# Optimization experiments

Hardware: AMD Instinct MI355X
Metric: run time of the kernel (lower is better)

## Reference

```python
import jax, jax.numpy as jnp
import numpy as np

EMBED_DIM = 1024
NUM_HEADS = 16
D_K = EMBED_DIM // NUM_HEADS


def setup_inputs() -> dict:
    key = jax.random.key(0)
    ks = jax.random.split(key, 5)
    s = 1.0 / np.sqrt(EMBED_DIM)  # roughly match nn.Linear init scale
    return {
        "x": jax.random.normal(ks[0], (2, 2048, EMBED_DIM), dtype=jnp.float32),
        "wq": jax.random.normal(ks[1], (EMBED_DIM, EMBED_DIM), dtype=jnp.float32) * s,
        "wk": jax.random.normal(ks[2], (EMBED_DIM, EMBED_DIM), dtype=jnp.float32) * s,
        "wv": jax.random.normal(ks[3], (EMBED_DIM, EMBED_DIM), dtype=jnp.float32) * s,
        "wo": jax.random.normal(ks[4], (EMBED_DIM, EMBED_DIM), dtype=jnp.float32) * s,
    }


def reference(x, wq, wk, wv, wo):
    b, s, e = x.shape
    # nn.Linear(bias=False): y = x @ W.T
    def split_heads(t):
        return t.reshape(b, s, NUM_HEADS, D_K).transpose(0, 2, 1, 3)  # [b,h,s,d]
    q = split_heads(x @ wq.T)
    k = split_heads(x @ wk.T)
    v = split_heads(x @ wv.T)
    scores = jnp.einsum("bhqd,bhkd->bhqk", q, k) / jnp.sqrt(jnp.float32(D_K))
    attn = jax.nn.softmax(scores, axis=-1)
    out = jnp.einsum("bhqk,bhkd->bhqd", attn, v)  # [b,h,s,d]
    out = out.transpose(0, 2, 1, 3).reshape(b, s, e)
    return out @ wo.T
```

## Files before the change

kernel.cpp:

```cpp
#include <hip/hip_runtime.h>
#include <stdint.h>

typedef unsigned short u16;
typedef float f32x4 __attribute__((ext_vector_type(4)));
typedef __bf16 bf16x8 __attribute__((ext_vector_type(8)));
typedef short s16x4 __attribute__((ext_vector_type(4)));

__device__ __forceinline__ u16 f2bf(float f) {
  union { float f; uint32_t u; } c; c.f = f;
  uint32_t u = c.u;
  u += 0x7fffu + ((u >> 16) & 1u);
  return (u16)(u >> 16);
}

__device__ __forceinline__ uint32_t pkbf(float a, float b) {
  union { float f; uint32_t u; } ua, ub; ua.f = a; ub.f = b;
  return __builtin_amdgcn_perm(ub.u, ua.u, 0x07060302u);
}

#define GLOAD_LDS16(g, l)                                                              \
  __builtin_amdgcn_global_load_lds((__attribute__((address_space(1))) void*)(g),       \
                                   (__attribute__((address_space(3))) void*)(l), 16, 0, 0)

__global__ __launch_bounds__(256) void cvt_all(const float* __restrict__ x,
                                               const float* __restrict__ wq,
                                               const float* __restrict__ wk,
                                               const float* __restrict__ wv,
                                               const float* __restrict__ wo,
                                               u16* __restrict__ xb,
                                               u16* __restrict__ wqkvb,
                                               u16* __restrict__ wob) {
  int bx = blockIdx.x;
  const float* src;
  u16* dst;
  int i;
  if (bx < 4096) {
    src = x; dst = xb; i = bx * 256 + threadIdx.x;
  } else {
    int r = bx - 4096;
    int w = r >> 10;
    i = (r & 1023) * 256 + threadIdx.x;
    if (w == 0)      { src = wq; dst = wqkvb; }
    else if (w == 1) { src = wk; dst = wqkvb + 1048576; }
    else if (w == 2) { src = wv; dst = wqkvb + 2097152; }
    else             { src = wo; dst = wob; }
  }
  const float4 v = ((const float4*)src)[i];
  ushort4 o;
  o.x = f2bf(v.x); o.y = f2bf(v.y); o.z = f2bf(v.z); o.w = f2bf(v.w);
  ((ushort4*)dst)[i] = o;
}

__global__ __launch_bounds__(256) void gemm_qkv(const u16* __restrict__ A,
                                                const u16* __restrict__ B,
                                                u16* __restrict__ QKb,
                                                u16* __restrict__ Vt) {
  const int K = 1024;
  __shared__ __align__(16) u16 sA[128 * 64];
  __shared__ __align__(16) u16 sB[128 * 64];
  const int tid = threadIdx.x;
  const int lane = tid & 63;
  const int wave = tid >> 6;
  const int quad = lane >> 4, l16 = lane & 15;
  const int wm = (wave >> 1) * 64, wn = (wave & 1) * 64;
  const int bm = blockIdx.y * 128, bn = blockIdx.x * 128;

  f32x4 acc[4][4];
#pragma unroll
  for (int i = 0; i < 4; i++)
#pragma unroll
    for (int j = 0; j < 4; j++) acc[i][j] = (f32x4){0.f, 0.f, 0.f, 0.f};

  for (int k0 = 0; k0 < K; k0 += 64) {
#pragma unroll
    for (int k2 = 0; k2 < 4; k2++) {
      int c = k2 * 256 + tid;
      int row = c >> 3, c8 = (c & 7) ^ (row & 7);
      GLOAD_LDS16(A + (size_t)(bm + row) * K + k0 + c8 * 8, (char*)sA + c * 16);
      GLOAD_LDS16(B + (size_t)(bn + row) * K + k0 + c8 * 8, (char*)sB + c * 16);
    }
    __syncthreads();
    bf16x8 af[4][2], bfr[4][2];
#pragma unroll
    for (int mt = 0; mt < 4; mt++)
#pragma unroll
      for (int kh = 0; kh < 2; kh++) {
        int ra = wm + mt * 16 + l16;
        af[mt][kh] = *(const bf16x8*)&sA[ra * 64 + (((kh * 4 + quad) ^ (ra & 7)) * 8)];
        int rb = wn + mt * 16 + l16;
        bfr[mt][kh] = *(const bf16x8*)&sB[rb * 64 + (((kh * 4 + quad) ^ (rb & 7)) * 8)];
      }
#pragma unroll
    for (int mt = 0; mt < 4; mt++)
#pragma unroll
      for (int nt = 0; nt < 4; nt++) {
        acc[mt][nt] = __builtin_amdgcn_mfma_f32_16x16x32_bf16(af[mt][0], bfr[nt][0], acc[mt][nt], 0, 0, 0);
        acc[mt][nt] = __builtin_amdgcn_mfma_f32_16x16x32_bf16(af[mt][1], bfr[nt][1], acc[mt][nt], 0, 0, 0);
      }
    __syncthreads();
  }

  if (blockIdx.x < 16) {
    const float qs = (blockIdx.x < 8) ? 0.18033688011f : 1.0f;
#pragma unroll
    for (int mt = 0; mt < 4; mt++)
#pragma unroll
      for (int nt = 0; nt < 4; nt++)
#pragma unroll
        for (int r = 0; r < 4; r++) {
          int row = bm + wm + mt * 16 + quad * 4 + r;
          int col = bn + wn + nt * 16 + l16;
          QKb[(size_t)row * 2048 + col] = f2bf(acc[mt][nt][r] * qs);
        }
  } else {
#pragma unroll
    for (int mt = 0; mt < 4; mt++)
#pragma unroll
      for (int nt = 0; nt < 4; nt++) {
        int hd = (bn - 2048) + wn + nt * 16 + l16;
        int tok = bm + wm + mt * 16 + quad * 4;
        ushort4 o;
        o.x = f2bf(acc[mt][nt][0]);
        o.y = f2bf(acc[mt][nt][1]);
        o.z = f2bf(acc[mt][nt][2]);
        o.w = f2bf(acc[mt][nt][3]);
        *(ushort4*)&Vt[(size_t)hd * 4096 + tok] = o;
      }
  }
}

__global__ __launch_bounds__(256, 2) void attn_fwd(const u16* __restrict__ QKb,
                                                   const u16* __restrict__ Vt,
                                                   u16* __restrict__ O) {
  const int bx = blockIdx.x;
  const int qt = bx >> 5;
  const int h  = (bx >> 1) & 15;
  const int b  = bx & 1;
  const int tid = threadIdx.x;
  const int lane = tid & 63;
  const int wave = tid >> 6;
  const int quad = lane >> 4, l16 = lane & 15;

  __shared__ __align__(16) u16 smem[16384];
  u16* sK0 = smem;
  u16* sK1 = smem + 4096;
  u16* sV0 = smem + 8192;
  u16* sV1 = smem + 12288;

  const int tok0 = b * 2048;
  const int q0 = qt * 128;
  const int colh = h * 64;

#pragma unroll
  for (int k2 = 0; k2 < 2; k2++) {
    int c = k2 * 256 + tid;
    int row = c >> 3, c8 = (c & 7) ^ (row & 7);
    GLOAD_LDS16(QKb + (size_t)(tok0 + q0 + row) * 2048 + colh + c8 * 8,
                (char*)sK1 + c * 16);
    GLOAD_LDS16(QKb + (size_t)(tok0 + q0 + 64 + row) * 2048 + colh + c8 * 8,
                (char*)sV1 + c * 16);
    GLOAD_LDS16(QKb + (size_t)(tok0 + row) * 2048 + 1024 + colh + c8 * 8,
                (char*)sK0 + c * 16);
    GLOAD_LDS16(Vt + (size_t)(colh + row) * 4096 + tok0 + c8 * 8,
                (char*)sV0 + c * 16);
  }
  __syncthreads();

  const u16* qreg = (wave < 2) ? sK1 : sV1;
  bf16x8 aq[2][2];
#pragma unroll
  for (int sub = 0; sub < 2; sub++)
#pragma unroll
    for (int kh = 0; kh < 2; kh++) {
      int r64 = (wave & 1) * 32 + sub * 16 + l16;
      aq[sub][kh] = *(const bf16x8*)&qreg[r64 * 64 + (((kh * 4 + quad) ^ (r64 & 7)) * 8)];
    }
  __syncthreads();

  f32x4 oacc[2][4];
  float lsum[2] = {0.f, 0.f};
#pragma unroll
  for (int sub = 0; sub < 2; sub++)
#pragma unroll
    for (int db = 0; db < 4; db++) oacc[sub][db] = (f32x4){0.f, 0.f, 0.f, 0.f};

  int p = 0;
  for (int it = 0; it < 32; ++it) {
    u16* sKc = p ? sK1 : sK0;
    u16* sVc = p ? sV1 : sV0;
    if (it < 31) {
      u16* sKn = p ? sK0 : sK1;
      u16* sVn = p ? sV0 : sV1;
      const int nkv = (it + 1) * 64;
#pragma unroll
      for (int k2 = 0; k2 < 2; k2++) {
        int c = k2 * 256 + tid;
        int row = c >> 3, c8 = (c & 7) ^ (row & 7);
        GLOAD_LDS16(QKb + (size_t)(tok0 + nkv + row) * 2048 + 1024 + colh + c8 * 8,
                    (char*)sKn + c * 16);
        GLOAD_LDS16(Vt + (size_t)(colh + row) * 4096 + tok0 + nkv + c8 * 8,
                    (char*)sVn + c * 16);
      }
    }

    bf16x8 kf[4][2];
#pragma unroll
    for (int nt = 0; nt < 4; nt++)
#pragma unroll
      for (int kh = 0; kh < 2; kh++) {
        int rr = nt * 16 + l16;
        kf[nt][kh] = *(const bf16x8*)&sKc[rr * 64 + (((kh * 4 + quad) ^ (rr & 7)) * 8)];
      }
    s16x4 vf[4][4];
#pragma unroll
    for (int db = 0; db < 4; db++)
#pragma unroll
      for (int nt = 0; nt < 4; nt++) {
        int row = db * 16 + l16;
        int c16 = (nt * 2 + (quad >> 1)) ^ (row & 7);
        vf[db][nt] = *(const s16x4*)&sVc[row * 64 + c16 * 8 + (quad & 1) * 4];
      }

#pragma unroll
    for (int sub = 0; sub < 2; sub++) {
      float e[4][4];
#pragma unroll
      for (int nt = 0; nt < 4; nt++) {
        f32x4 c = (f32x4){0.f, 0.f, 0.f, 0.f};
        c = __builtin_amdgcn_mfma_f32_16x16x32_bf16(kf[nt][0], aq[sub][0], c, 0, 0, 0);
        c = __builtin_amdgcn_mfma_f32_16x16x32_bf16(kf[nt][1], aq[sub][1], c, 0, 0, 0);
#pragma unroll
        for (int r = 0; r < 4; r++) e[nt][r] = __builtin_amdgcn_exp2f(c[r]);
        lsum[sub] += (e[nt][0] + e[nt][1]) + (e[nt][2] + e[nt][3]);
      }
#pragma unroll
      for (int nt = 0; nt < 4; nt++) {
        union { uint32_t u[2]; s16x4 v; } bb;
        bb.u[0] = pkbf(e[nt][0], e[nt][1]);
        bb.u[1] = pkbf(e[nt][2], e[nt][3]);
#pragma unroll
        for (int db = 0; db < 4; db++)
          oacc[sub][db] = __builtin_amdgcn_mfma_f32_16x16x16bf16_1k(vf[db][nt], bb.v, oacc[sub][db], 0, 0, 0);
      }
    }
    __syncthreads();
    p ^= 1;
  }

#pragma unroll
  for (int sub = 0; sub < 2; sub++) {
    float v = lsum[sub];
    v += __shfl_xor(v, 16, 64);
    v += __shfl_xor(v, 32, 64);
    lsum[sub] = 1.0f / v;
  }

  u16* sT = smem + wave * 2176;
#pragma unroll
  for (int sub = 0; sub < 2; sub++)
#pragma unroll
    for (int db = 0; db < 4; db++)
#pragma unroll
      for (int r = 0; r < 4; r++)
        sT[(sub * 16 + l16) * 68 + db * 16 + quad * 4 + r] = f2bf(oacc[sub][db][r] * lsum[sub]);
#pragma unroll
  for (int k = 0; k < 4; k++) {
    int qrow = k * 8 + (lane >> 3);
    int cch = lane & 7;
    uint4 vrow = *(const uint4*)&sT[qrow * 68 + cch * 8];
    int tokr = tok0 + q0 + wave * 32 + qrow;
    *(uint4*)&O[(size_t)tokr * 1024 + colh + cch * 8] = vrow;
  }
}

__global__ __launch_bounds__(256) void gemm_out(const u16* __restrict__ A,
                                                const u16* __restrict__ B,
                                                float* __restrict__ C) {
  const int N = 1024, K = 1024;
  __shared__ __align__(16) u16 sA[128 * 64];
  __shared__ __align__(16) u16 sB[64 * 64];
  const int tid = threadIdx.x;
  const int lane = tid & 63;
  const int wave = tid >> 6;
  const int quad = lane >> 4, l16 = lane & 15;
  const int wm = (wave >> 1) * 64, wn = (wave & 1) * 32;
  const int bm = blockIdx.y * 128, bn = blockIdx.x * 64;

  f32x4 acc[4][2];
#pragma unroll
  for (int i = 0; i < 4; i++)
#pragma unroll
    for (int j = 0; j < 2; j++) acc[i][j] = (f32x4){0.f, 0.f, 0.f, 0.f};

  for (int k0 = 0; k0 < K; k0 += 64) {
#pragma unroll
    for (int k2 = 0; k2 < 4; k2++) {
      int c = k2 * 256 + tid;
      int row = c >> 3, c8 = (c & 7) ^ (row & 7);
      GLOAD_LDS16(A + (size_t)(bm + row) * K + k0 + c8 * 8, (char*)sA + c * 16);
    }
#pragma unroll
    for (int k2 = 0; k2 < 2; k2++) {
      int c = k2 * 256 + tid;
      int row = c >> 3, c8 = (c & 7) ^ (row & 7);
      GLOAD_LDS16(B + (size_t)(bn + row) * K + k0 + c8 * 8, (char*)sB + c * 16);
    }
    __syncthreads();
    bf16x8 af[4][2], bfr[2][2];
#pragma unroll
    for (int mt = 0; mt < 4; mt++)
#pragma unroll
      for (int kh = 0; kh < 2; kh++) {
        int ra = wm + mt * 16 + l16;
        af[mt][kh] = *(const bf16x8*)&sA[ra * 64 + (((kh * 4 + quad) ^ (ra & 7)) * 8)];
      }
#pragma unroll
    for (int nt = 0; nt < 2; nt++)
#pragma unroll
      for (int kh = 0; kh < 2; kh++) {
        int rb = wn + nt * 16 + l16;
        bfr[nt][kh] = *(const bf16x8*)&sB[rb * 64 + (((kh * 4 + quad) ^ (rb & 7)) * 8)];
      }
#pragma unroll
    for (int mt = 0; mt < 4; mt++)
#pragma unroll
      for (int nt = 0; nt < 2; nt++) {
        acc[mt][nt] = __builtin_amdgcn_mfma_f32_16x16x32_bf16(af[mt][0], bfr[nt][0], acc[mt][nt], 0, 0, 0);
        acc[mt][nt] = __builtin_amdgcn_mfma_f32_16x16x32_bf16(af[mt][1], bfr[nt][1], acc[mt][nt], 0, 0, 0);
      }
    __syncthreads();
  }

#pragma unroll
  for (int mt = 0; mt < 4; mt++)
#pragma unroll
    for (int nt = 0; nt < 2; nt++)
#pragma unroll
      for (int r = 0; r < 4; r++) {
        int row = bm + wm + mt * 16 + quad * 4 + r;
        int col = bn + wn + nt * 16 + l16;
        C[(size_t)row * N + col] = acc[mt][nt][r];
      }
}

extern "C" void kernel_launch(void* const* d_in, const int* in_sizes, int n_in,
                              void* d_out, int out_size, void* d_ws, size_t ws_size,
                              hipStream_t stream) {
  const float* x  = (const float*)d_in[0];
  const float* wq = (const float*)d_in[1];
  const float* wk = (const float*)d_in[2];
  const float* wv = (const float*)d_in[3];
  const float* wo = (const float*)d_in[4];
  float* out = (float*)d_out;
  char* ws = (char*)d_ws;
  const size_t MB = 1u << 20;

  u16* xb    = (u16*)(ws);
  u16* wqkvb = (u16*)(ws + 8 * MB);
  u16* wob   = (u16*)(ws + 14 * MB);
  u16* QKb   = (u16*)(ws + 16 * MB);
  u16* Vtb   = (u16*)(ws + 32 * MB);
  u16* Ob    = xb;

  cvt_all<<<8192, 256, 0, stream>>>(x, wq, wk, wv, wo, xb, wqkvb, wob);

  gemm_qkv<<<dim3(24, 32), 256, 0, stream>>>(xb, wqkvb, QKb, Vtb);

  attn_fwd<<<512, 256, 0, stream>>>(QKb, Vtb, Ob);

  gemm_out<<<dim3(16, 32), 256, 0, stream>>>(Ob, wob, out);
}
```

Baseline: 186.5 us.

## Triple-buffer LDS pipelines in GEMMs and attention with async load waits

Both GEMMs now use a 3-stage LDS ring with 32-wide K slices, prefetching two stages ahead. Each stage waits on a partial vmcnt and issues a single barrier, replacing the load-then-syncthreads double sync per iteration. The attention kernel gets the same treatment: a 3-deep K/V ring, a dedicated Q buffer, and s_setprio raised around MFMA groups. The goal is to hide global-to-LDS latency behind compute. The cost is more LDS per block, which may reduce occupancy, and correctness now depends on the hand-counted vmcnt values and on the ordering implied by the single barrier.

```diff
diff --git a/kernel.cpp b/kernel.cpp
--- a/kernel.cpp
+++ b/kernel.cpp
@@ -51,13 +51,13 @@
   ((ushort4*)dst)[i] = o;
 }
 
-__global__ __launch_bounds__(256) void gemm_qkv(const u16* __restrict__ A,
-                                                const u16* __restrict__ B,
-                                                u16* __restrict__ QKb,
-                                                u16* __restrict__ Vt) {
+__global__ __launch_bounds__(256, 3) void gemm_qkv(const u16* __restrict__ A,
+                                                   const u16* __restrict__ B,
+                                                   u16* __restrict__ QKb,
+                                                   u16* __restrict__ Vt) {
   const int K = 1024;
-  __shared__ __align__(16) u16 sA[128 * 64];
-  __shared__ __align__(16) u16 sB[128 * 64];
+  __shared__ __align__(16) u16 sA[3 * 4096];
+  __shared__ __align__(16) u16 sB[3 * 4096];
   const int tid = threadIdx.x;
   const int lane = tid & 63;
   const int wave = tid >> 6;
@@ -71,34 +71,54 @@
 #pragma unroll
     for (int j = 0; j < 4; j++) acc[i][j] = (f32x4){0.f, 0.f, 0.f, 0.f};
 
-  for (int k0 = 0; k0 < K; k0 += 64) {
-#pragma unroll
-    for (int k2 = 0; k2 < 4; k2++) {
-      int c = k2 * 256 + tid;
-      int row = c >> 3, c8 = (c & 7) ^ (row & 7);
-      GLOAD_LDS16(A + (size_t)(bm + row) * K + k0 + c8 * 8, (char*)sA + c * 16);
-      GLOAD_LDS16(B + (size_t)(bn + row) * K + k0 + c8 * 8, (char*)sB + c * 16);
-    }
-    __syncthreads();
-    bf16x8 af[4][2], bfr[4][2];
+#define QKV_STAGE(t, bi)                                                           \
+  {                                                                                \
+    const int k0s = (t) * 32;                                                      \
+    char* dA = (char*)(sA + (bi) * 4096);                                          \
+    char* dB = (char*)(sB + (bi) * 4096);                                          \
+    _Pragma("unroll")                                                              \
+    for (int k2 = 0; k2 < 2; k2++) {                                               \
+      int u = k2 * 256 + tid;                                                      \
+      int row = u >> 2, c4 = (u & 3) ^ (row & 3);                                  \
+      GLOAD_LDS16(A + (size_t)(bm + row) * K + k0s + c4 * 8, dA + u * 16);         \
+      GLOAD_LDS16(B + (size_t)(bn + row) * K + k0s + c4 * 8, dB + u * 16);         \
+    }                                                                              \
+  }
+
+  QKV_STAGE(0, 0);
+  QKV_STAGE(1, 1);
+
+  int cur = 0, stg = 2;
+  for (int T = 0; T < 32; ++T) {
+    if (T < 31) asm volatile("s_waitcnt vmcnt(4)" ::: "memory");
+    else        asm volatile("s_waitcnt vmcnt(0)" ::: "memory");
+    __builtin_amdgcn_s_barrier();
+    asm volatile("" ::: "memory");
+    if (T < 30) QKV_STAGE(T + 2, stg);
+
+    const u16* cA = sA + cur * 4096;
+    const u16* cB = sB + cur * 4096;
+    bf16x8 af[4], bfr[4];
+#pragma unroll
+    for (int mt = 0; mt < 4; mt++) {
+      int ra = wm + mt * 16 + l16;
+      af[mt] = *(const bf16x8*)&cA[ra * 32 + ((quad ^ (ra & 3)) * 8)];
+    }
+#pragma unroll
+    for (int nt = 0; nt < 4; nt++) {
+      int rb = wn + nt * 16 + l16;
+      bfr[nt] = *(const bf16x8*)&cB[rb * 32 + ((quad ^ (rb & 3)) * 8)];
+    }
 #pragma unroll
     for (int mt = 0; mt < 4; mt++)
 #pragma unroll
-      for (int kh = 0; kh < 2; kh++) {
-        int ra = wm + mt * 16 + l16;
-        af[mt][kh] = *(const bf16x8*)&sA[ra * 64 + (((kh * 4 + quad) ^ (ra & 7)) * 8)];
-        int rb = wn + mt * 16 + l16;
-        bfr[mt][kh] = *(const bf16x8*)&sB[rb * 64 + (((kh * 4 + quad) ^ (rb & 7)) * 8)];
-      }
-#pragma unroll
-    for (int mt = 0; mt < 4; mt++)
-#pragma unroll
-      for (int nt = 0; nt < 4; nt++) {
-        acc[mt][nt] = __builtin_amdgcn_mfma_f32_16x16x32_bf16(af[mt][0], bfr[nt][0], acc[mt][nt], 0, 0, 0);
-        acc[mt][nt] = __builtin_amdgcn_mfma_f32_16x16x32_bf16(af[mt][1], bfr[nt][1], acc[mt][nt], 0, 0, 0);
-      }
-    __syncthreads();
-  }
+      for (int nt = 0; nt < 4; nt++)
+        acc[mt][nt] = __builtin_amdgcn_mfma_f32_16x16x32_bf16(af[mt], bfr[nt], acc[mt][nt], 0, 0, 0);
+
+    cur = (cur == 2) ? 0 : cur + 1;
+    stg = (stg == 2) ? 0 : stg + 1;
+  }
+#undef QKV_STAGE
 
   if (blockIdx.x < 16) {
     const float qs = (blockIdx.x < 8) ? 0.18033688011f : 1.0f;
@@ -141,41 +161,46 @@
   const int wave = tid >> 6;
   const int quad = lane >> 4, l16 = lane & 15;
 
-  __shared__ __align__(16) u16 smem[16384];
-  u16* sK0 = smem;
-  u16* sK1 = smem + 4096;
-  u16* sV0 = smem + 8192;
-  u16* sV1 = smem + 12288;
+  __shared__ __align__(16) u16 smem[32768];
+  u16* sQ = smem;
+  u16* sK = smem + 8192;
+  u16* sV = smem + 20480;
 
   const int tok0 = b * 2048;
   const int q0 = qt * 128;
   const int colh = h * 64;
 
 #pragma unroll
-  for (int k2 = 0; k2 < 2; k2++) {
+  for (int k2 = 0; k2 < 4; k2++) {
     int c = k2 * 256 + tid;
     int row = c >> 3, c8 = (c & 7) ^ (row & 7);
     GLOAD_LDS16(QKb + (size_t)(tok0 + q0 + row) * 2048 + colh + c8 * 8,
-                (char*)sK1 + c * 16);
-    GLOAD_LDS16(QKb + (size_t)(tok0 + q0 + 64 + row) * 2048 + colh + c8 * 8,
-                (char*)sV1 + c * 16);
-    GLOAD_LDS16(QKb + (size_t)(tok0 + row) * 2048 + 1024 + colh + c8 * 8,
-                (char*)sK0 + c * 16);
-    GLOAD_LDS16(Vt + (size_t)(colh + row) * 4096 + tok0 + c8 * 8,
-                (char*)sV0 + c * 16);
-  }
-  __syncthreads();
-
-  const u16* qreg = (wave < 2) ? sK1 : sV1;
+                (char*)sQ + c * 16);
+  }
+#pragma unroll
+  for (int t = 0; t < 2; t++) {
+#pragma unroll
+    for (int k2 = 0; k2 < 2; k2++) {
+      int c = k2 * 256 + tid;
+      int row = c >> 3, c8 = (c & 7) ^ (row & 7);
+      GLOAD_LDS16(QKb + (size_t)(tok0 + t * 64 + row) * 2048 + 1024 + colh + c8 * 8,
+                  (char*)(sK + t * 4096) + c * 16);
+      GLOAD_LDS16(Vt + (size_t)(colh + row) * 4096 + tok0 + t * 64 + c8 * 8,
+                  (char*)(sV + t * 4096) + c * 16);
+    }
+  }
+  asm volatile("s_waitcnt vmcnt(8)" ::: "memory");
+  __builtin_amdgcn_s_barrier();
+  asm volatile("" ::: "memory");
+
   bf16x8 aq[2][2];
 #pragma unroll
   for (int sub = 0; sub < 2; sub++)
 #pragma unroll
     for (int kh = 0; kh < 2; kh++) {
-      int r64 = (wave & 1) * 32 + sub * 16 + l16;
-      aq[sub][kh] = *(const bf16x8*)&qreg[r64 * 64 + (((kh * 4 + quad) ^ (r64 & 7)) * 8)];
-    }
-  __syncthreads();
+      int rq = wave * 32 + sub * 16 + l16;
+      aq[sub][kh] = *(const bf16x8*)&sQ[rq * 64 + (((kh * 4 + quad) ^ (rq & 7)) * 8)];
+    }
 
   f32x4 oacc[2][4];
   float lsum[2] = {0.f, 0.f};
@@ -184,24 +209,28 @@
 #pragma unroll
     for (int db = 0; db < 4; db++) oacc[sub][db] = (f32x4){0.f, 0.f, 0.f, 0.f};
 
-  int p = 0;
+  int cur = 0, stg = 2;
   for (int it = 0; it < 32; ++it) {
-    u16* sKc = p ? sK1 : sK0;
-    u16* sVc = p ? sV1 : sV0;
-    if (it < 31) {
-      u16* sKn = p ? sK0 : sK1;
-      u16* sVn = p ? sV0 : sV1;
-      const int nkv = (it + 1) * 64;
+    if (it < 31) asm volatile("s_waitcnt vmcnt(4)" ::: "memory");
+    else         asm volatile("s_waitcnt vmcnt(0)" ::: "memory");
+    __builtin_amdgcn_s_barrier();
+    asm volatile("" ::: "memory");
+    if (it < 30) {
+      const int nkv = (it + 2) * 64;
+      char* sKn = (char*)(sK + stg * 4096);
+      char* sVn = (char*)(sV + stg * 4096);
 #pragma unroll
       for (int k2 = 0; k2 < 2; k2++) {
         int c = k2 * 256 + tid;
         int row = c >> 3, c8 = (c & 7) ^ (row & 7);
         GLOAD_LDS16(QKb + (size_t)(tok0 + nkv + row) * 2048 + 1024 + colh + c8 * 8,
-                    (char*)sKn + c * 16);
+                    sKn + c * 16);
         GLOAD_LDS16(Vt + (size_t)(colh + row) * 4096 + tok0 + nkv + c8 * 8,
-                    (char*)sVn + c * 16);
-      }
-    }
+                    sVn + c * 16);
+      }
+    }
+    const u16* sKc = sK + cur * 4096;
+    const u16* sVc = sV + cur * 4096;
 
     bf16x8 kf[4][2];
 #pragma unroll
@@ -227,8 +256,10 @@
 #pragma unroll
       for (int nt = 0; nt < 4; nt++) {
         f32x4 c = (f32x4){0.f, 0.f, 0.f, 0.f};
+        __builtin_amdgcn_s_setprio(1);
         c = __builtin_amdgcn_mfma_f32_16x16x32_bf16(kf[nt][0], aq[sub][0], c, 0, 0, 0);
         c = __builtin_amdgcn_mfma_f32_16x16x32_bf16(kf[nt][1], aq[sub][1], c, 0, 0, 0);
+        __builtin_amdgcn_s_setprio(0);
 #pragma unroll
         for (int r = 0; r < 4; r++) e[nt][r] = __builtin_amdgcn_exp2f(c[r]);
         lsum[sub] += (e[nt][0] + e[nt][1]) + (e[nt][2] + e[nt][3]);
@@ -238,13 +269,15 @@
         union { uint32_t u[2]; s16x4 v; } bb;
         bb.u[0] = pkbf(e[nt][0], e[nt][1]);
         bb.u[1] = pkbf(e[nt][2], e[nt][3]);
+        __builtin_amdgcn_s_setprio(1);
 #pragma unroll
         for (int db = 0; db < 4; db++)
           oacc[sub][db] = __builtin_amdgcn_mfma_f32_16x16x16bf16_1k(vf[db][nt], bb.v, oacc[sub][db], 0, 0, 0);
-      }
-    }
-    __syncthreads();
-    p ^= 1;
+        __builtin_amdgcn_s_setprio(0);
+      }
+    }
+    cur = (cur == 2) ? 0 : cur + 1;
+    stg = (stg == 2) ? 0 : stg + 1;
   }
 
 #pragma unroll
@@ -277,8 +310,8 @@
                                                 const u16* __restrict__ B,
                                                 float* __restrict__ C) {
   const int N = 1024, K = 1024;
-  __shared__ __align__(16) u16 sA[128 * 64];
-  __shared__ __align__(16) u16 sB[64 * 64];
+  __shared__ __align__(16) u16 sA[3 * 4096];
+  __shared__ __align__(16) u16 sB[3 * 2048];
   const int tid = threadIdx.x;
   const int lane = tid & 63;
   const int wave = tid >> 6;
@@ -292,44 +325,58 @@
 #pragma unroll
     for (int j = 0; j < 2; j++) acc[i][j] = (f32x4){0.f, 0.f, 0.f, 0.f};
 
-  for (int k0 = 0; k0 < K; k0 += 64) {
-#pragma unroll
-    for (int k2 = 0; k2 < 4; k2++) {
-      int c = k2 * 256 + tid;
-      int row = c >> 3, c8 = (c & 7) ^ (row & 7);
-      GLOAD_LDS16(A + (size_t)(bm + row) * K + k0 + c8 * 8, (char*)sA + c * 16);
-    }
-#pragma unroll
-    for (int k2 = 0; k2 < 2; k2++) {
-      int c = k2 * 256 + tid;
-      int row = c >> 3, c8 = (c & 7) ^ (row & 7);
-      GLOAD_LDS16(B + (size_t)(bn + row) * K + k0 + c8 * 8, (char*)sB + c * 16);
-    }
-    __syncthreads();
-    bf16x8 af[4][2], bfr[2][2];
+#define OUT_STAGE(t, bi)                                                           \
+  {                                                                                \
+    const int k0s = (t) * 32;                                                      \
+    char* dA = (char*)(sA + (bi) * 4096);                                          \
+    char* dB = (char*)(sB + (bi) * 2048);                                          \
+    _Pragma("unroll")                                                              \
+    for (int k2 = 0; k2 < 2; k2++) {                                               \
+      int u = k2 * 256 + tid;                                                      \
+      int row = u >> 2, c4 = (u & 3) ^ (row & 3);                                  \
+      GLOAD_LDS16(A + (size_t)(bm + row) * K + k0s + c4 * 8, dA + u * 16);         \
+    }                                                                              \
+    {                                                                              \
+      int u = tid;                                                                 \
+      int row = u >> 2, c4 = (u & 3) ^ (row & 3);                                  \
+      GLOAD_LDS16(B + (size_t)(bn + row) * K + k0s + c4 * 8, dB + u * 16);         \
+    }                                                                              \
+  }
+
+  OUT_STAGE(0, 0);
+  OUT_STAGE(1, 1);
+
+  int cur = 0, stg = 2;
+  for (int T = 0; T < 32; ++T) {
+    if (T < 31) asm volatile("s_waitcnt vmcnt(3)" ::: "memory");
+    else        asm volatile("s_waitcnt vmcnt(0)" ::: "memory");
+    __builtin_amdgcn_s_barrier();
+    asm volatile("" ::: "memory");
+    if (T < 30) OUT_STAGE(T + 2, stg);
+
+    const u16* cA = sA + cur * 4096;
+    const u16* cB = sB + cur * 2048;
+    bf16x8 af[4], bfr[2];
+#pragma unroll
+    for (int mt = 0; mt < 4; mt++) {
+      int ra = wm + mt * 16 + l16;
+      af[mt] = *(const bf16x8*)&cA[ra * 32 + ((quad ^ (ra & 3)) * 8)];
+    }
+#pragma unroll
+    for (int nt = 0; nt < 2; nt++) {
+      int rb = wn + nt * 16 + l16;
+      bfr[nt] = *(const bf16x8*)&cB[rb * 32 + ((quad ^ (rb & 3)) * 8)];
+    }
 #pragma unroll
     for (int mt = 0; mt < 4; mt++)
 #pragma unroll
-      for (int kh = 0; kh < 2; kh++) {
-        int ra = wm + mt * 16 + l16;
-        af[mt][kh] = *(const bf16x8*)&sA[ra * 64 + (((kh * 4 + quad) ^ (ra & 7)) * 8)];
-      }
-#pragma unroll
-    for (int nt = 0; nt < 2; nt++)
-#pragma unroll
-      for (int kh = 0; kh < 2; kh++) {
-        int rb = wn + nt * 16 + l16;
-        bfr[nt][kh] = *(const bf16x8*)&sB[rb * 64 + (((kh * 4 + quad) ^ (rb & 7)) * 8)];
-      }
-#pragma unroll
-    for (int mt = 0; mt < 4; mt++)
-#pragma unroll
-      for (int nt = 0; nt < 2; nt++) {
-        acc[mt][nt] = __builtin_amdgcn_mfma_f32_16x16x32_bf16(af[mt][0], bfr[nt][0], acc[mt][nt], 0, 0, 0);
-        acc[mt][nt] = __builtin_amdgcn_mfma_f32_16x16x32_bf16(af[mt][1], bfr[nt][1], acc[mt][nt], 0, 0, 0);
-      }
-    __syncthreads();
-  }
+      for (int nt = 0; nt < 2; nt++)
+        acc[mt][nt] = __builtin_amdgcn_mfma_f32_16x16x32_bf16(af[mt], bfr[nt], acc[mt][nt], 0, 0, 0);
+
+    cur = (cur == 2) ? 0 : cur + 1;
+    stg = (stg == 2) ? 0 : stg + 1;
+  }
+#undef OUT_STAGE
 
 #pragma unroll
   for (int mt = 0; mt < 4; mt++)
```

Result: no change. 187.6 us (+0.6%).
